# Kernel optimization log

Measured on AMD Instinct MI355X. Metric: run time of the kernel, lower is better.

The kernel has to match this reference:

```python
import jax, jax.numpy as jnp
import numpy as np

HEADS = 8
GROUPS = 32   # Group_cnt in the source
WIN = 16      # config.local_window_size


def _gn_nc(x, groups, eps):
    # group_norm on [N, C] (affine=False)
    N, C = x.shape
    xg = x.reshape(N, groups, C // groups)
    m = xg.mean(axis=2, keepdims=True)
    v = xg.var(axis=2, keepdims=True)
    return ((xg - m) / jnp.sqrt(v + eps)).reshape(N, C)


def _gn_nchw(x, groups, eps):
    # group_norm on [B, C, H, W] (affine=False)
    B, C, H, W = x.shape
    xg = x.reshape(B, groups, C // groups, H, W)
    m = xg.mean(axis=(2, 3, 4), keepdims=True)
    v = xg.var(axis=(2, 3, 4), keepdims=True)
    return ((xg - m) / jnp.sqrt(v + eps)).reshape(B, C, H, W)


def _conv3x3(x, w, b=None):
    y = jax.lax.conv_general_dilated(x, w, (1, 1), 'SAME',
                                     dimension_numbers=('NCHW', 'OIHW', 'NCHW'))
    return y if b is None else y + b[None, :, None, None]


def _forward(x, temb, conv1_w, conv1_b, conv2_w, g_diff, g_res, g2, g3,
             qkv2_w, qkv2_b, out2_w, qkv3_w, qkv3_b, out3_w,
             lsa_qkv_w, lsa_out_w):
    # ---- Residual_Block (layer1) ----
    h = _gn_nchw(x, GROUPS, 1e-6)
    h = _conv3x3(h, conv1_w, conv1_b)
    h = h + g_diff * temb[:, :, None, None]      # gate_diffusion (ReZero-style gate)
    h = jax.nn.silu(h)
    h = _gn_nchw(h, GROUPS, 1e-6)
    h = _conv3x3(h, conv2_w)
    h = _gn_nchw(h, GROUPS, 1e-6)
    x = x + g_res * h                            # gate_residual

    B, C, Fq, T = x.shape
    Dh = C // HEADS
    scale = 1.0 / jnp.sqrt(jnp.float32(Dh))      # (F/heads)**0.5 divisor

    # ---- SelfAttention over frequency axis (layer2): batch B*T, seq Fq ----
    xf = x.transpose(0, 3, 2, 1).reshape(B * T, Fq, C)
    qkv = xf @ qkv2_w + qkv2_b                   # [B*T, Fq, 3C]
    q, k, v = [t.reshape(B * T, Fq, HEADS, Dh) for t in jnp.split(qkv, 3, axis=-1)]
    p = jax.nn.softmax(jnp.einsum('bLhf,blhf->bLlh', q, k) * scale, axis=2)
    y = jnp.einsum('blhf,bLlh->bLhf', v, p).reshape(B * T, Fq, C) @ out2_w
    y = _gn_nc(y.reshape(-1, C), GROUPS, 1e-5).reshape(B * T, Fq, C)
    xf = xf + g2 * y                             # gate2

    # ---- GlobalAttention over time axis (layer3): batch B*Fq, seq T ----
    xt = xf.reshape(B, T, Fq, C).transpose(0, 2, 1, 3).reshape(B * Fq, T, C)
    qkv = xt @ qkv3_w + qkv3_b
    q, k, v = [t.reshape(B * Fq, T, HEADS, Dh) for t in jnp.split(qkv, 3, axis=-1)]
    p = jax.nn.softmax(jnp.einsum('bhf,blhf->blh', q.mean(axis=1), k) * scale, axis=1)
    y = jnp.einsum('blhf,blh->bhf', v, p).reshape(B * Fq, C) @ out3_w
    y = _gn_nc(y, GROUPS, 1e-5).reshape(B * Fq, 1, C)
    xt = xt + g3 * y                             # gate3, broadcast over T
    x = xt.reshape(B, Fq, T, C).transpose(0, 3, 1, 2)

    # ---- LSA_block (layer4): pre-norm local windowed attention along T, residual ----
    h = _gn_nchw(x, GROUPS, 1e-5)
    h = h.transpose(0, 2, 3, 1).reshape(B * Fq, T, C)
    nw = T // WIN
    qkv = (h @ lsa_qkv_w).reshape(B * Fq, nw, WIN, 3 * C)
    q, k, v = [t.reshape(B * Fq, nw, WIN, HEADS, Dh) for t in jnp.split(qkv, 3, axis=-1)]
    p = jax.nn.softmax(jnp.einsum('nwqhd,nwkhd->nwqkh', q, k) * scale, axis=3)
    o = jnp.einsum('nwqkh,nwkhd->nwqhd', p, v).reshape(B * Fq, T, C) @ lsa_out_w
    return x + o.reshape(B, Fq, T, C).transpose(0, 3, 1, 2)


def setup_inputs() -> dict:
    key = jax.random.key(0)
    ks = jax.random.split(key, 10)
    B, C, Fq, T = 4, 256, 64, 256
    w = lambda k, s: jax.random.normal(k, s, dtype=jnp.float32) * 0.02
    return {
        'x': jax.random.normal(ks[0], (B, C, Fq, T), dtype=jnp.float32),
        'temb': jax.random.normal(ks[1], (B, C), dtype=jnp.float32),
        'conv1_w': w(ks[2], (C, C, 3, 3)),
        'conv1_b': jnp.zeros((C,), jnp.float32),
        'conv2_w': w(ks[3], (C, C, 3, 3)),
        'g_diff': jnp.full((1,), 0.5, jnp.float32),
        'g_res': jnp.full((1,), 0.5, jnp.float32),
        'g2': jnp.full((1,), 0.5, jnp.float32),
        'g3': jnp.full((1,), 0.5, jnp.float32),
        'qkv2_w': w(ks[4], (C, 3 * C)),
        'qkv2_b': jnp.zeros((3 * C,), jnp.float32),
        'out2_w': w(ks[5], (C, C)),
        'qkv3_w': w(ks[6], (C, 3 * C)),
        'qkv3_b': jnp.zeros((3 * C,), jnp.float32),
        'out3_w': w(ks[7], (C, C)),
        'lsa_qkv_w': w(ks[8], (C, 3 * C)),
        'lsa_out_w': w(ks[9], (C, C)),
    }


def reference(x, temb, conv1_w, conv1_b, conv2_w, g_diff, g_res, g2, g3,
              qkv2_w, qkv2_b, out2_w, qkv3_w, qkv3_b, out3_w,
              lsa_qkv_w, lsa_out_w):
    return _forward(x, temb, conv1_w, conv1_b, conv2_w, g_diff, g_res, g2, g3,
                    qkv2_w, qkv2_b, out2_w, qkv3_w, qkv3_b, out3_w,
                    lsa_qkv_w, lsa_out_w)
```

## Files before the change

kernel.cpp:

```cpp
#include <hip/hip_runtime.h>

#define NN 16777216
#define CC 256
#define FF 64
#define TT 256

typedef short v8s __attribute__((ext_vector_type(8)));
typedef float v4f __attribute__((ext_vector_type(4)));

__device__ __forceinline__ unsigned short f2bf(float f) {
  unsigned u = __float_as_uint(f);
  u += 0x7fff + ((u >> 16) & 1);
  return (unsigned short)(u >> 16);
}
__device__ __forceinline__ float bf2f(unsigned short h) {
  return __uint_as_float(((unsigned)h) << 16);
}
__device__ __forceinline__ unsigned packbf2(float a, float b) {
  return (unsigned)f2bf(a) | ((unsigned)f2bf(b) << 16);
}
__device__ __forceinline__ void unpack8(uint4 u, float* d) {
  d[0] = __uint_as_float(u.x << 16); d[1] = __uint_as_float(u.x & 0xffff0000u);
  d[2] = __uint_as_float(u.y << 16); d[3] = __uint_as_float(u.y & 0xffff0000u);
  d[4] = __uint_as_float(u.z << 16); d[5] = __uint_as_float(u.z & 0xffff0000u);
  d[6] = __uint_as_float(u.w << 16); d[7] = __uint_as_float(u.w & 0xffff0000u);
}

__device__ __forceinline__ void blockReduce2(float& a, float& b, float* sbuf) {
  #pragma unroll
  for (int off = 32; off > 0; off >>= 1) {
    a += __shfl_down(a, off, 64);
    b += __shfl_down(b, off, 64);
  }
  int w = threadIdx.x >> 6;
  if ((threadIdx.x & 63) == 0) { sbuf[w] = a; sbuf[4 + w] = b; }
  __syncthreads();
  if (threadIdx.x == 0) {
    a = sbuf[0] + sbuf[1] + sbuf[2] + sbuf[3];
    b = sbuf[4] + sbuf[5] + sbuf[6] + sbuf[7];
  }
}

__global__ void prep_all_k(const float* __restrict__ c1w, const float* __restrict__ c2w,
    const float* __restrict__ q2w, const float* __restrict__ o2w, const float* __restrict__ q3w,
    const float* __restrict__ lqw, const float* __restrict__ low,
    unsigned short* __restrict__ WB1, unsigned short* __restrict__ WB2,
    unsigned short* __restrict__ Q2T, unsigned short* __restrict__ O2T,
    unsigned short* __restrict__ Q3T, unsigned short* __restrict__ LQT,
    unsigned short* __restrict__ LOT, float* __restrict__ stats) {
  long s = (long)blockIdx.x * 256 + threadIdx.x;
  if (s < 1024) { stats[s] = 0.f; return; }
  s -= 1024;
  if (s < 589824) {
    int co = (int)(s / 2304), r = (int)(s % 2304);
    int ci = r / 9, tap = r % 9;
    WB1[(tap * 256 + co) * 256 + ci] = f2bf(c1w[s]);
    return;
  }
  s -= 589824;
  if (s < 589824) {
    int co = (int)(s / 2304), r = (int)(s % 2304);
    int ci = r / 9, tap = r % 9;
    WB2[(tap * 256 + co) * 256 + ci] = f2bf(c2w[s]);
    return;
  }
  s -= 589824;
  if (s < 196608) { int k = (int)(s / 768), n = (int)(s % 768); Q2T[n * 256 + k] = f2bf(q2w[s]); return; }
  s -= 196608;
  if (s < 65536)  { int k = (int)(s / 256), n = (int)(s % 256); O2T[n * 256 + k] = f2bf(o2w[s]); return; }
  s -= 65536;
  if (s < 196608) { int k = (int)(s / 768), n = (int)(s % 768); Q3T[n * 256 + k] = f2bf(q3w[s]); return; }
  s -= 196608;
  if (s < 196608) { int k = (int)(s / 768), n = (int)(s % 768); LQT[n * 256 + k] = f2bf(lqw[s]); return; }
  s -= 196608;
  if (s < 65536)  { int k = (int)(s / 256), n = (int)(s % 256); LOT[n * 256 + k] = f2bf(low[s]); return; }
}

__global__ __launch_bounds__(256) void gn_stats_contig(const float* __restrict__ src, float* __restrict__ stats) {
  __shared__ float sbuf[8];
  int grp = blockIdx.x >> 3, chunk = blockIdx.x & 7;
  const float4* p = (const float4*)src + grp * 32768 + chunk * 4096;
  float s = 0.f, ss = 0.f;
  for (int i = threadIdx.x; i < 4096; i += 256) {
    float4 v = p[i];
    s += v.x + v.y + v.z + v.w;
    ss += v.x * v.x + v.y * v.y + v.z * v.z + v.w * v.w;
  }
  blockReduce2(s, ss, sbuf);
  if (threadIdx.x == 0) { atomicAdd(&stats[grp], s); atomicAdd(&stats[128 + grp], ss); }
}

__global__ __launch_bounds__(256) void gn_apply_tr_k(const float* __restrict__ src,
    const float* __restrict__ stats, unsigned short* __restrict__ XC, float eps) {
  __shared__ float sT[32][33];
  int bx = blockIdx.x;
  int r = bx >> 6;
  int c0 = ((bx >> 3) & 7) * 32;
  int t0 = (bx & 7) * 32;
  int b = r >> 6, f = r & 63;
  int tl = threadIdx.x & 31, tr = threadIdx.x >> 5;
  #pragma unroll
  for (int i = 0; i < 4; ++i) {
    int c = c0 + tr + i * 8;
    int grp = b * 32 + (c >> 3);
    float mean = stats[grp] * (1.f / 131072.f);
    float var = stats[128 + grp] * (1.f / 131072.f) - mean * mean;
    float rv = rsqrtf(var + eps);
    float v = src[((b * 256 + c) * 64 + f) * 256 + t0 + tl];
    sT[tr + i * 8][tl] = (v - mean) * rv;
  }
  __syncthreads();
  #pragma unroll
  for (int i = 0; i < 4; ++i) {
    int t = t0 + tr + i * 8;
    XC[(((size_t)(b * 64 + f)) * 256 + t) * 256 + c0 + tl] = f2bf(sT[tl][tr + i * 8]);
  }
}

__global__ __launch_bounds__(256) void gn_tr_resid_k(const float* __restrict__ h,
    const float* __restrict__ x, const float* __restrict__ stats,
    const float* __restrict__ gate, float* __restrict__ XF, float eps) {
  __shared__ float sT[32][33];
  int bx = blockIdx.x;
  int r = bx >> 6;
  int c0 = ((bx >> 3) & 7) * 32;
  int t0 = (bx & 7) * 32;
  int b = r >> 6, f = r & 63;
  int tl = threadIdx.x & 31, tr = threadIdx.x >> 5;
  float g = gate[0];
  #pragma unroll
  for (int i = 0; i < 4; ++i) {
    int c = c0 + tr + i * 8;
    int grp = b * 32 + (c >> 3);
    float mean = stats[grp] * (1.f / 131072.f);
    float var = stats[128 + grp] * (1.f / 131072.f) - mean * mean;
    float rv = rsqrtf(var + eps);
    int idx = ((b * 256 + c) * 64 + f) * 256 + t0 + tl;
    sT[tr + i * 8][tl] = x[idx] + g * (h[idx] - mean) * rv;
  }
  __syncthreads();
  #pragma unroll
  for (int i = 0; i < 4; ++i) {
    int t = t0 + tr + i * 8;
    XF[(((size_t)(b * 256 + t)) * 64 + f) * 256 + c0 + tl] = sT[tl][tr + i * 8];
  }
}

__global__ __launch_bounds__(256, 4) void conv3x3_mfma_k(const unsigned short* __restrict__ XC,
    const unsigned short* __restrict__ wb, const float* __restrict__ bias,
    const float* __restrict__ temb, const float* __restrict__ gd,
    float* __restrict__ out, float* __restrict__ ostats, int mode) {
  __shared__ __align__(16) unsigned short sIn[258][40];
  __shared__ __align__(16) unsigned short sW[3][64][40];
  int f  = blockIdx.x;
  int b  = blockIdx.y >> 2;
  int co0 = (blockIdx.y & 3) * 64;
  int tid = threadIdx.x;
  int wave = tid >> 6, lane = tid & 63;
  int lm = lane & 15, quad = lane >> 4;
  int w64 = wave * 64;
  v4f acc[4][4];
  #pragma unroll
  for (int i = 0; i < 4; ++i)
    #pragma unroll
    for (int j = 0; j < 4; ++j) acc[i][j] = (v4f)(0.f);

  for (int ci0 = 0; ci0 < 256; ci0 += 32) {
    for (int df = 0; df < 3; ++df) {
      __syncthreads();
      for (int s = tid; s < 1032; s += 256) {
        int tl = s >> 2, part = s & 3;
        int fi = f + df - 1, tg = tl - 1;
        uint4 val = make_uint4(0, 0, 0, 0);
        if (fi >= 0 && fi < 64 && tg >= 0 && tg < 256)
          val = *(const uint4*)&XC[(((size_t)(b * 64 + fi)) * 256 + tg) * 256 + ci0 + part * 8];
        *(uint4*)&sIn[tl][part * 8] = val;
      }
      for (int s = tid; s < 768; s += 256) {
        int tap3 = s >> 8, r = s & 255;
        int co = r >> 2, part = r & 3;
        *(uint4*)&sW[tap3][co][part * 8] =
            *(const uint4*)&wb[((size_t)((df * 3 + tap3) * 256) + co0 + co) * 256 + ci0 + part * 8];
      }
      __syncthreads();
      #pragma unroll
      for (int dt = 0; dt < 3; ++dt) {
        v8s A[4];
        #pragma unroll
        for (int mt = 0; mt < 4; ++mt)
          A[mt] = *(const v8s*)&sIn[w64 + mt * 16 + lm + dt][quad * 8];
        #pragma unroll
        for (int nt = 0; nt < 4; ++nt) {
          v8s B = *(const v8s*)&sW[dt][nt * 16 + lm][quad * 8];
          #pragma unroll
          for (int mt = 0; mt < 4; ++mt)
            acc[mt][nt] = __builtin_amdgcn_mfma_f32_16x16x32_bf16(A[mt], B, acc[mt][nt], 0, 0, 0);
        }
      }
    }
  }
  __syncthreads();
  float* sStat = (float*)sIn;
  float gdv = mode ? gd[0] : 0.f;
  float sch, qch;
  #pragma unroll
  for (int nt = 0; nt < 4; ++nt) {
    int co = co0 + nt * 16 + lm;
    float bb = 0.f;
    if (mode) bb = bias[co] + gdv * temb[b * 256 + co];
    sch = 0.f; qch = 0.f;
    #pragma unroll
    for (int mt = 0; mt < 4; ++mt) {
      int t = w64 + mt * 16 + quad * 4;
      float v0 = acc[mt][nt][0] + bb, v1 = acc[mt][nt][1] + bb;
      float v2 = acc[mt][nt][2] + bb, v3 = acc[mt][nt][3] + bb;
      if (mode) {
        v0 = v0 / (1.f + expf(-v0)); v1 = v1 / (1.f + expf(-v1));
        v2 = v2 / (1.f + expf(-v2)); v3 = v3 / (1.f + expf(-v3));
      }
      float4 o; o.x = v0; o.y = v1; o.z = v2; o.w = v3;
      *(float4*)&out[(((size_t)b * 256 + co) * 64 + f) * 256 + t] = o;
      sch += v0 + v1 + v2 + v3;
      qch += v0 * v0 + v1 * v1 + v2 * v2 + v3 * v3;
    }
    sch += __shfl_xor(sch, 16); qch += __shfl_xor(qch, 16);
    sch += __shfl_xor(sch, 32); qch += __shfl_xor(qch, 32);
    if (quad == 0) {
      sStat[((wave * 4 + nt) * 16 + lm) * 2]     = sch;
      sStat[((wave * 4 + nt) * 16 + lm) * 2 + 1] = qch;
    }
  }
  __syncthreads();
  if (tid < 64) {
    int c = tid;
    int nt = c >> 4, lmm = c & 15;
    float s = 0.f, q = 0.f;
    #pragma unroll
    for (int w = 0; w < 4; ++w) {
      s += sStat[((w * 4 + nt) * 16 + lmm) * 2];
      q += sStat[((w * 4 + nt) * 16 + lmm) * 2 + 1];
    }
    s += __shfl_xor(s, 1); q += __shfl_xor(q, 1);
    s += __shfl_xor(s, 2); q += __shfl_xor(q, 2);
    s += __shfl_xor(s, 4); q += __shfl_xor(q, 4);
    if ((c & 7) == 0) {
      int g = (co0 + c) >> 3;
      atomicAdd(&ostats[b * 32 + g], s);
      atomicAdd(&ostats[128 + b * 32 + g], q);
    }
  }
}

__global__ __launch_bounds__(256) void gemm_af32_k(const float* __restrict__ A, int lda,
    const unsigned short* __restrict__ BT, const float* __restrict__ bias,
    unsigned short* __restrict__ Cb, int ldc,
    const float* __restrict__ gstats, int growbase, float eps) {
  __shared__ __align__(16) unsigned short sA[128][40];
  __shared__ __align__(16) unsigned short sB[128][40];
  int n0 = blockIdx.x * 128, m0 = blockIdx.y * 128;
  int tid = threadIdx.x;
  int wave = tid >> 6, lane = tid & 63;
  int wm = wave >> 1, wn = wave & 1;
  int lm = lane & 15, quad = lane >> 4;
  v4f acc[4][4];
  #pragma unroll
  for (int i = 0; i < 4; ++i)
    #pragma unroll
    for (int j = 0; j < 4; ++j) acc[i][j] = (v4f)(0.f);

  for (int k0 = 0; k0 < 256; k0 += 32) {
    __syncthreads();
    #pragma unroll
    for (int i = 0; i < 4; ++i) {
      int s = tid + i * 256;
      int row = s >> 3, k4 = s & 7;
      float4 av = *(const float4*)&A[(size_t)(m0 + row) * lda + k0 + k4 * 4];
      if (gstats) {
        int grp = ((growbase + m0 + row) >> 14) * 32 + ((k0 + k4 * 4) >> 3);
        float mean = gstats[grp] * (1.f / 131072.f);
        float var = gstats[128 + grp] * (1.f / 131072.f) - mean * mean;
        float rr = rsqrtf(var + eps);
        av.x = (av.x - mean) * rr; av.y = (av.y - mean) * rr;
        av.z = (av.z - mean) * rr; av.w = (av.w - mean) * rr;
      }
      *(uint2*)&sA[row][k4 * 4] = make_uint2(packbf2(av.x, av.y), packbf2(av.z, av.w));
    }
    #pragma unroll
    for (int i = 0; i < 2; ++i) {
      int s = tid + i * 256;
      int n = s >> 2, part = s & 3;
      *(uint4*)&sB[n][part * 8] = *(const uint4*)&BT[(size_t)(n0 + n) * 256 + k0 + part * 8];
    }
    __syncthreads();
    v8s Af[4];
    #pragma unroll
    for (int mt = 0; mt < 4; ++mt)
      Af[mt] = *(const v8s*)&sA[wm * 64 + mt * 16 + lm][quad * 8];
    #pragma unroll
    for (int nt = 0; nt < 4; ++nt) {
      v8s Bf = *(const v8s*)&sB[wn * 64 + nt * 16 + lm][quad * 8];
      #pragma unroll
      for (int mt = 0; mt < 4; ++mt)
        acc[mt][nt] = __builtin_amdgcn_mfma_f32_16x16x32_bf16(Af[mt], Bf, acc[mt][nt], 0, 0, 0);
    }
  }
  #pragma unroll
  for (int nt = 0; nt < 4; ++nt) {
    int col = n0 + wn * 64 + nt * 16 + lm;
    float bb = bias ? bias[col] : 0.f;
    #pragma unroll
    for (int mt = 0; mt < 4; ++mt) {
      int row = m0 + wm * 64 + mt * 16 + quad * 4;
      #pragma unroll
      for (int r = 0; r < 4; ++r)
        Cb[(size_t)(row + r) * ldc + col] = f2bf(acc[mt][nt][r] + bb);
    }
  }
}

__global__ __launch_bounds__(256) void gemm_abf16_k(const unsigned short* __restrict__ A, int lda,
    const unsigned short* __restrict__ BT,
    const float* __restrict__ xfin, float* __restrict__ xtout, int rowbase,
    unsigned short* __restrict__ Cb, int ldc, const float* __restrict__ gate) {
  __shared__ __align__(16) unsigned short sA[128][40];
  __shared__ __align__(16) unsigned short sB[128][40];
  int n0 = blockIdx.x * 128, m0 = blockIdx.y * 128;
  int tid = threadIdx.x;
  int wave = tid >> 6, lane = tid & 63;
  int wm = wave >> 1, wn = wave & 1;
  int lm = lane & 15, quad = lane >> 4;
  v4f acc[4][4];
  #pragma unroll
  for (int i = 0; i < 4; ++i)
    #pragma unroll
    for (int j = 0; j < 4; ++j) acc[i][j] = (v4f)(0.f);

  for (int k0 = 0; k0 < 256; k0 += 32) {
    __syncthreads();
    #pragma unroll
    for (int i = 0; i < 2; ++i) {
      int s = tid + i * 256;
      int row = s >> 2, part = s & 3;
      *(uint4*)&sA[row][part * 8] = *(const uint4*)&A[(size_t)(m0 + row) * lda + k0 + part * 8];
      *(uint4*)&sB[row][part * 8] = *(const uint4*)&BT[(size_t)(n0 + row) * 256 + k0 + part * 8];
    }
    __syncthreads();
    v8s Af[4];
    #pragma unroll
    for (int mt = 0; mt < 4; ++mt)
      Af[mt] = *(const v8s*)&sA[wm * 64 + mt * 16 + lm][quad * 8];
    #pragma unroll
    for (int nt = 0; nt < 4; ++nt) {
      v8s Bf = *(const v8s*)&sB[wn * 64 + nt * 16 + lm][quad * 8];
      #pragma unroll
      for (int mt = 0; mt < 4; ++mt)
        acc[mt][nt] = __builtin_amdgcn_mfma_f32_16x16x32_bf16(Af[mt], Bf, acc[mt][nt], 0, 0, 0);
    }
  }
  if (xtout) {
    float g = gate[0];
    #pragma unroll
    for (int mt = 0; mt < 4; ++mt) {
      int rowb = m0 + wm * 64 + mt * 16 + quad * 4;
      #pragma unroll
      for (int r = 0; r < 4; ++r) {
        int rowl = rowb + r;
        int rowg = rowbase + rowl;
        int b = rowg >> 14, t = (rowg >> 6) & 255, fq = rowg & 63;
        size_t xtrow = (size_t)((b * 64 + fq) * 256 + t) * 256;
        #pragma unroll
        for (int nt = 0; nt < 4; ++nt) {
          float v = acc[mt][nt][r];
          float s = v, q = v * v;
          s += __shfl_xor(s, 1); q += __shfl_xor(q, 1);
          s += __shfl_xor(s, 2); q += __shfl_xor(q, 2);
          s += __shfl_xor(s, 4); q += __shfl_xor(q, 4);
          float m = s * 0.125f;
          float var = q * 0.125f - m * m;
          float norm = (v - m) * rsqrtf(var + 1e-5f);
          int col = n0 + wn * 64 + nt * 16 + lm;
          xtout[xtrow + col] = xfin[(size_t)rowl * 256 + col] + g * norm;
        }
      }
    }
  } else {
    #pragma unroll
    for (int nt = 0; nt < 4; ++nt) {
      int col = n0 + wn * 64 + nt * 16 + lm;
      #pragma unroll
      for (int mt = 0; mt < 4; ++mt) {
        int row = m0 + wm * 64 + mt * 16 + quad * 4;
        #pragma unroll
        for (int r = 0; r < 4; ++r)
          Cb[(size_t)(row + r) * ldc + col] = f2bf(acc[mt][nt][r]);
      }
    }
  }
}

__global__ __launch_bounds__(256) void gemm_k(const float* __restrict__ A, int lda,
    const float* __restrict__ Bm, int N, const float* __restrict__ bias,
    float* __restrict__ Cm, int ldc, int gn) {
  __shared__ __align__(16) float sA[16][64];
  __shared__ __align__(16) float sB[16][64];
  int n0 = blockIdx.x * 64, m0 = blockIdx.y * 64;
  int tid = threadIdx.x;
  int tx = tid & 15, ty = tid >> 4;
  int arow = m0 + (tid >> 2), acol = (tid & 3) * 4;
  int brow = tid >> 4, bcol = (tid & 15) * 4;
  float acc[4][4] = {};
  for (int k0 = 0; k0 < 256; k0 += 16) {
    __syncthreads();
    float4 av = *(const float4*)&A[(size_t)arow * lda + k0 + acol];
    sA[acol + 0][tid >> 2] = av.x;
    sA[acol + 1][tid >> 2] = av.y;
    sA[acol + 2][tid >> 2] = av.z;
    sA[acol + 3][tid >> 2] = av.w;
    *(float4*)&sB[brow][bcol] = *(const float4*)&Bm[(k0 + brow) * N + n0 + bcol];
    __syncthreads();
    #pragma unroll
    for (int kk = 0; kk < 16; ++kk) {
      float4 a = *(const float4*)&sA[kk][ty * 4];
      float4 b = *(const float4*)&sB[kk][tx * 4];
      float aa[4] = {a.x, a.y, a.z, a.w};
      float bb[4] = {b.x, b.y, b.z, b.w};
      #pragma unroll
      for (int i = 0; i < 4; ++i)
        #pragma unroll
        for (int j = 0; j < 4; ++j)
          acc[i][j] += aa[i] * bb[j];
    }
  }
  #pragma unroll
  for (int i = 0; i < 4; ++i) {
    float m = 0.f, rv = 1.f;
    if (gn) {
      float s = acc[i][0] + acc[i][1] + acc[i][2] + acc[i][3];
      float q = acc[i][0] * acc[i][0] + acc[i][1] * acc[i][1]
              + acc[i][2] * acc[i][2] + acc[i][3] * acc[i][3];
      s += __shfl_xor(s, 1); q += __shfl_xor(q, 1);
      m = s * 0.125f;
      float var = q * 0.125f - m * m;
      rv = rsqrtf(var + 1e-5f);
    }
    #pragma unroll
    for (int j = 0; j < 4; ++j) {
      int n = n0 + tx * 4 + j;
      float v = acc[i][j];
      if (gn) v = (v - m) * rv;
      else if (bias) v += bias[n];
      Cm[(size_t)(m0 + ty * 4 + i) * ldc + n] = v;
    }
  }
}

__global__ __launch_bounds__(256) void final_out_k(const float* __restrict__ XT,
    const unsigned short* __restrict__ O2b, float* __restrict__ out, int rbase) {
  __shared__ float sT[32][33];
  int bx = blockIdx.x;
  int rl = bx >> 6;
  int t0 = ((bx >> 3) & 7) * 32;
  int c0 = (bx & 7) * 32;
  int rg = rbase + rl;
  int b = rg >> 6, f = rg & 63;
  int tc = threadIdx.x & 31, tr = threadIdx.x >> 5;
  #pragma unroll
  for (int i = 0; i < 4; ++i) {
    int t = t0 + tr + i * 8;
    sT[tr + i * 8][tc] = XT[(size_t)rg * 65536 + t * 256 + c0 + tc]
                       + bf2f(O2b[(size_t)rl * 65536 + t * 256 + c0 + tc]);
  }
  __syncthreads();
  #pragma unroll
  for (int i = 0; i < 4; ++i) {
    int c = c0 + tr + i * 8;
    out[((b * CC + c) * FF + f) * TT + t0 + tc] = sT[tc][tr + i * 8];
  }
}

__global__ __launch_bounds__(256) void attn2_mfma_k(unsigned short* __restrict__ Q) {
  __shared__ __align__(16) unsigned short sP[4][64][72];
  __shared__ __align__(16) unsigned short sVt[4][32][72];
  int bt = blockIdx.x;
  int tid = threadIdx.x;
  int wave = tid >> 6, lane = tid & 63;
  int lm = lane & 15, quad = lane >> 4;
  const float scale = 0.17677669529663687f;
  size_t rowbase = (size_t)bt * 64;
  unsigned short (*P)[72] = sP[wave];
  unsigned short (*Vt)[72] = sVt[wave];
  #pragma unroll
  for (int hh = 0; hh < 2; ++hh) {
    int h = wave * 2 + hh;
    int hoff = h * 32;
    v8s Af[4], Bf[4];
    #pragma unroll
    for (int mt = 0; mt < 4; ++mt)
      Af[mt] = *(const v8s*)&Q[(rowbase + mt * 16 + lm) * 768 + hoff + quad * 8];
    #pragma unroll
    for (int nt = 0; nt < 4; ++nt)
      Bf[nt] = *(const v8s*)&Q[(rowbase + nt * 16 + lm) * 768 + 256 + hoff + quad * 8];
    v4f S[4][4];
    #pragma unroll
    for (int mt = 0; mt < 4; ++mt)
      #pragma unroll
      for (int nt = 0; nt < 4; ++nt)
        S[mt][nt] = __builtin_amdgcn_mfma_f32_16x16x32_bf16(Af[mt], Bf[nt], (v4f)(0.f), 0, 0, 0);
    #pragma unroll
    for (int part = 0; part < 4; ++part) {
      uint4 u = *(const uint4*)&Q[(rowbase + lane) * 768 + 512 + hoff + part * 8];
      unsigned short* up = (unsigned short*)&u;
      #pragma unroll
      for (int j = 0; j < 8; ++j) Vt[part * 8 + j][lane] = up[j];
    }
    float inv[4][4];
    #pragma unroll
    for (int mt = 0; mt < 4; ++mt) {
      #pragma unroll
      for (int r = 0; r < 4; ++r) {
        float v0 = S[mt][0][r] * scale, v1 = S[mt][1][r] * scale;
        float v2 = S[mt][2][r] * scale, v3 = S[mt][3][r] * scale;
        float mx = fmaxf(fmaxf(v0, v1), fmaxf(v2, v3));
        mx = fmaxf(mx, __shfl_xor(mx, 1));
        mx = fmaxf(mx, __shfl_xor(mx, 2));
        mx = fmaxf(mx, __shfl_xor(mx, 4));
        mx = fmaxf(mx, __shfl_xor(mx, 8));
        float e0 = __expf(v0 - mx), e1 = __expf(v1 - mx);
        float e2 = __expf(v2 - mx), e3 = __expf(v3 - mx);
        float sm = e0 + e1 + e2 + e3;
        sm += __shfl_xor(sm, 1);
        sm += __shfl_xor(sm, 2);
        sm += __shfl_xor(sm, 4);
        sm += __shfl_xor(sm, 8);
        inv[mt][r] = 1.f / sm;
        int row = mt * 16 + quad * 4 + r;
        P[row][lm]      = f2bf(e0);
        P[row][16 + lm] = f2bf(e1);
        P[row][32 + lm] = f2bf(e2);
        P[row][48 + lm] = f2bf(e3);
      }
    }
    v8s Ap[4][2], Bv[2][2];
    #pragma unroll
    for (int mt = 0; mt < 4; ++mt)
      #pragma unroll
      for (int kc = 0; kc < 2; ++kc)
        Ap[mt][kc] = *(const v8s*)&P[mt * 16 + lm][kc * 32 + quad * 8];
    #pragma unroll
    for (int nd = 0; nd < 2; ++nd)
      #pragma unroll
      for (int kc = 0; kc < 2; ++kc)
        Bv[nd][kc] = *(const v8s*)&Vt[nd * 16 + lm][kc * 32 + quad * 8];
    #pragma unroll
    for (int mt = 0; mt < 4; ++mt) {
      #pragma unroll
      for (int nd = 0; nd < 2; ++nd) {
        v4f O = (v4f)(0.f);
        O = __builtin_amdgcn_mfma_f32_16x16x32_bf16(Ap[mt][0], Bv[nd][0], O, 0, 0, 0);
        O = __builtin_amdgcn_mfma_f32_16x16x32_bf16(Ap[mt][1], Bv[nd][1], O, 0, 0, 0);
        #pragma unroll
        for (int r = 0; r < 4; ++r)
          P[mt * 16 + quad * 4 + r][nd * 16 + lm] = f2bf(O[r] * inv[mt][r]);
      }
    }
    #pragma unroll
    for (int part = 0; part < 4; ++part) {
      uint4 u = *(const uint4*)&P[lane][part * 8];
      *(uint4*)&Q[(rowbase + lane) * 768 + hoff + part * 8] = u;
    }
  }
}

__global__ __launch_bounds__(256) void attn3_k(const unsigned short* __restrict__ Q3,
                                               float* __restrict__ y3, int bf_base) {
  __shared__ float sQp[64][33];
  __shared__ float sqm[32];
  __shared__ float sp[256];
  __shared__ float sred[256];
  int bfl = blockIdx.x >> 3, h = blockIdx.x & 7;
  int tid = threadIdx.x;
  int tq = tid >> 2, c4 = tid & 3;
  int d8 = c4 * 8;
  const float scale = 0.17677669529663687f;
  size_t rowbase = (size_t)bfl * 256;
  {
    float a[8] = {};
    #pragma unroll
    for (int i = 0; i < 4; ++i) {
      int t = i * 64 + tq;
      float v[8];
      unpack8(*(const uint4*)&Q3[(rowbase + t) * 768 + h * 32 + d8], v);
      #pragma unroll
      for (int j = 0; j < 8; ++j) a[j] += v[j];
    }
    #pragma unroll
    for (int j = 0; j < 8; ++j) sQp[tq][d8 + j] = a[j];
  }
  __syncthreads();
  if (tid < 32) {
    float m = 0.f;
    for (int g = 0; g < 64; ++g) m += sQp[g][tid];
    sqm[tid] = m * (1.f / 256.f);
  }
  __syncthreads();
  {
    float dot = 0.f;
    #pragma unroll
    for (int p = 0; p < 4; ++p) {
      float v[8];
      unpack8(*(const uint4*)&Q3[(rowbase + tid) * 768 + 256 + h * 32 + p * 8], v);
      #pragma unroll
      for (int j = 0; j < 8; ++j) dot += sqm[p * 8 + j] * v[j];
    }
    sp[tid] = dot * scale;
    sred[tid] = sp[tid];
  }
  __syncthreads();
  for (int st = 128; st > 0; st >>= 1) { if (tid < st) sred[tid] = fmaxf(sred[tid], sred[tid + st]); __syncthreads(); }
  float mx = sred[0];
  __syncthreads();
  float e = expf(sp[tid] - mx);
  sred[tid] = e;
  __syncthreads();
  for (int st = 128; st > 0; st >>= 1) { if (tid < st) sred[tid] += sred[tid + st]; __syncthreads(); }
  float rinv = 1.f / sred[0];
  sp[tid] = e * rinv;
  __syncthreads();
  {
    float a[8] = {};
    #pragma unroll
    for (int i = 0; i < 4; ++i) {
      int t = i * 64 + tq;
      float w = sp[t];
      float v[8];
      unpack8(*(const uint4*)&Q3[(rowbase + t) * 768 + 512 + h * 32 + d8], v);
      #pragma unroll
      for (int j = 0; j < 8; ++j) a[j] += w * v[j];
    }
    #pragma unroll
    for (int j = 0; j < 8; ++j) sQp[tq][d8 + j] = a[j];
  }
  __syncthreads();
  if (tid < 32) {
    float o = 0.f;
    for (int g = 0; g < 64; ++g) o += sQp[g][tid];
    y3[(size_t)(bf_base + bfl) * 256 + h * 32 + tid] = o;
  }
}

__global__ __launch_bounds__(256) void lsa_attn_k(unsigned short* __restrict__ Q4) {
  __shared__ __align__(16) float sX[16][772];
  __shared__ float sS[8][16][17];
  __shared__ float sInv[8][16];
  int bfl = blockIdx.x >> 4, w = blockIdx.x & 15;
  int tid = threadIdx.x;
  size_t rb = ((size_t)(bfl * 256 + w * 16)) * 768;
  for (int s = tid; s < 1536; s += 256) {
    int t = s / 96, c8 = (s - t * 96) * 8;
    unpack8(*(const uint4*)&Q4[rb + t * 768 + c8], &sX[t][c8]);
  }
  __syncthreads();
  const float scale = 0.17677669529663687f;
  #pragma unroll
  for (int rep = 0; rep < 8; ++rep) {
    int idx = tid + rep * 256;
    int h = idx >> 8, q = (idx >> 4) & 15, k = idx & 15;
    float dot = 0.f;
    const float* qp = &sX[q][h * 32];
    const float* kp = &sX[k][256 + h * 32];
    for (int d = 0; d < 32; ++d) dot += qp[d] * kp[d];
    sS[h][q][k] = dot * scale;
  }
  __syncthreads();
  if (tid < 128) {
    int h = tid >> 4, q = tid & 15;
    float mx = -1e30f;
    for (int k = 0; k < 16; ++k) mx = fmaxf(mx, sS[h][q][k]);
    float sum = 0.f;
    for (int k = 0; k < 16; ++k) { float e = expf(sS[h][q][k] - mx); sS[h][q][k] = e; sum += e; }
    sInv[h][q] = 1.f / sum;
  }
  __syncthreads();
  #pragma unroll
  for (int rep = 0; rep < 8; ++rep) {
    int idx = tid + rep * 256;
    int t = idx >> 7, c2 = (idx & 127) * 2;
    int h = c2 >> 5;
    float a0 = 0.f, a1 = 0.f;
    for (int k = 0; k < 16; ++k) {
      float p = sS[h][t][k];
      a0 += p * sX[k][512 + c2];
      a1 += p * sX[k][512 + c2 + 1];
    }
    float riv = sInv[h][t];
    *(unsigned*)&Q4[rb + t * 768 + c2] = packbf2(a0 * riv, a1 * riv);
  }
}

__global__ __launch_bounds__(256) void bcast_add_k(float* __restrict__ XT, const float* __restrict__ y3n,
                                                   const float* __restrict__ gate) {
  int i4 = blockIdx.x * 256 + threadIdx.x;
  int flat = i4 * 4;
  int r = flat >> 16, c = flat & 255;
  float g = gate[0];
  float4 v = ((float4*)XT)[i4];
  float4 a = *(const float4*)&y3n[r * 256 + c];
  v.x += g * a.x; v.y += g * a.y; v.z += g * a.z; v.w += g * a.w;
  ((float4*)XT)[i4] = v;
}

__global__ __launch_bounds__(256) void gn_stats_xt_k(const float* __restrict__ X, float* __restrict__ stats) {
  __shared__ float sbuf[8];
  int bx = blockIdx.x;
  int b = bx >> 11, g = (bx >> 6) & 31, f = bx & 63;
  size_t base = (size_t)(b * 64 + f) * 65536 + g * 8;
  float s = 0.f, ss = 0.f;
  for (int i = threadIdx.x; i < 2048; i += 256) {
    int t = i >> 3, c = i & 7;
    float v = X[base + t * 256 + c];
    s += v; ss += v * v;
  }
  blockReduce2(s, ss, sbuf);
  if (threadIdx.x == 0) { atomicAdd(&stats[b * 32 + g], s); atomicAdd(&stats[128 + b * 32 + g], ss); }
}

extern "C" void kernel_launch(void* const* d_in, const int* in_sizes, int n_in,
                              void* d_out, int out_size, void* d_ws, size_t ws_size,
                              hipStream_t stream) {
  (void)in_sizes; (void)n_in; (void)out_size;
  const float* x        = (const float*)d_in[0];
  const float* temb     = (const float*)d_in[1];
  const float* conv1_w  = (const float*)d_in[2];
  const float* conv1_b  = (const float*)d_in[3];
  const float* conv2_w  = (const float*)d_in[4];
  const float* g_diff   = (const float*)d_in[5];
  const float* g_res    = (const float*)d_in[6];
  const float* g2       = (const float*)d_in[7];
  const float* g3       = (const float*)d_in[8];
  const float* qkv2_w   = (const float*)d_in[9];
  const float* qkv2_b   = (const float*)d_in[10];
  const float* out2_w   = (const float*)d_in[11];
  const float* qkv3_w   = (const float*)d_in[12];
  const float* qkv3_b   = (const float*)d_in[13];
  const float* out3_w   = (const float*)d_in[14];
  const float* lsa_qkv_w = (const float*)d_in[15];
  const float* lsa_out_w = (const float*)d_in[16];
  float* out = (float*)d_out;
  float* ws = (float*)d_ws;

  int NCHv = 4;
  {
    auto need = [](int nch) -> size_t {
      size_t rows = 65536 / nch;
      size_t uslots = rows * 512;
      if (uslots < 8388608) uslots = 8388608;
      return 4ull * ((size_t)NN + uslots + 950272 + 198000);
    };
    if (ws_size >= need(1)) NCHv = 1;
    else if (ws_size >= need(2)) NCHv = 2;
  }
  const size_t rows = 65536 / NCHv;

  float* W = ws;
  float* U = ws + (size_t)NN;
  unsigned short* XC  = (unsigned short*)U;
  unsigned short* QB  = (unsigned short*)U;
  unsigned short* O2B = (unsigned short*)(U + rows * 384);
  size_t uslots = rows * 512; if (uslots < 8388608) uslots = 8388608;
  float* WREG = U + uslots;
  unsigned short* WB1   = (unsigned short*)WREG;
  unsigned short* WB2   = WB1 + 589824;
  unsigned short* QKV2T = WB2 + 589824;
  unsigned short* OUT2T = QKV2T + 196608;
  unsigned short* QKV3T = OUT2T + 65536;
  unsigned short* LSAQT = QKV3T + 196608;
  unsigned short* LSAOT = LSAQT + 196608;
  float* Y3    = WREG + 950272;
  float* Y3O   = Y3 + 65536;
  float* Y3N   = Y3O + 65536;
  float* STATS = Y3N + 65536;
  float* ST0 = STATS, *ST1 = STATS + 256, *ST2 = STATS + 512, *ST3 = STATS + 768;
  float* D = out;

  dim3 b256(256);
  prep_all_k<<<7428, b256, 0, stream>>>(conv1_w, conv2_w, qkv2_w, out2_w, qkv3_w,
                                        lsa_qkv_w, lsa_out_w,
                                        WB1, WB2, QKV2T, OUT2T, QKV3T, LSAQT, LSAOT, STATS);

  gn_stats_contig<<<1024, b256, 0, stream>>>(x, ST0);
  gn_apply_tr_k<<<16384, b256, 0, stream>>>(x, ST0, XC, 1e-6f);
  conv3x3_mfma_k<<<dim3(64, 16), b256, 0, stream>>>(XC, WB1, conv1_b, temb, g_diff, W, ST1, 1);
  gn_apply_tr_k<<<16384, b256, 0, stream>>>(W, ST1, XC, 1e-6f);
  conv3x3_mfma_k<<<dim3(64, 16), b256, 0, stream>>>(XC, WB2, nullptr, nullptr, nullptr, W, ST2, 0);
  gn_tr_resid_k<<<16384, b256, 0, stream>>>(W, x, ST2, g_res, D, 1e-6f);

  for (int c = 0; c < NCHv; ++c) {
    float* XFr = D + (size_t)c * rows * 256;
    gemm_af32_k<<<dim3(6, rows / 128), b256, 0, stream>>>(XFr, 256, QKV2T, qkv2_b, QB, 768, nullptr, 0, 0.f);
    attn2_mfma_k<<<rows / 64, b256, 0, stream>>>(QB);
    gemm_abf16_k<<<dim3(2, rows / 128), b256, 0, stream>>>(QB, 768, OUT2T,
                                                           XFr, W, (int)(c * rows),
                                                           nullptr, 256, g2);
  }

  for (int c = 0; c < NCHv; ++c) {
    const float* XTr = W + (size_t)c * rows * 256;
    gemm_af32_k<<<dim3(6, rows / 128), b256, 0, stream>>>(XTr, 256, QKV3T, qkv3_b, QB, 768, nullptr, 0, 0.f);
    attn3_k<<<(rows / 256) * 8, b256, 0, stream>>>(QB, Y3, c * (int)(rows / 256));
  }
  gemm_k<<<dim3(4, 4), b256, 0, stream>>>(Y3, 256, out3_w, 256, nullptr, Y3N, 256, 1);
  bcast_add_k<<<16384, b256, 0, stream>>>(W, Y3N, g3);

  gn_stats_xt_k<<<8192, b256, 0, stream>>>(W, ST3);
  for (int c = 0; c < NCHv; ++c) {
    const float* XTr = W + (size_t)c * rows * 256;
    gemm_af32_k<<<dim3(6, rows / 128), b256, 0, stream>>>(XTr, 256, LSAQT, nullptr, QB, 768,
                                                          ST3, (int)(c * rows), 1e-5f);
    lsa_attn_k<<<(rows / 256) * 16, b256, 0, stream>>>(QB);
    gemm_abf16_k<<<dim3(2, rows / 128), b256, 0, stream>>>(QB, 768, LSAOT,
                                                           nullptr, nullptr, 0,
                                                           O2B, 256, nullptr);
    final_out_k<<<(rows / 256) * 64, b256, 0, stream>>>(W, O2B, out, c * (int)(rows / 256));
  }
}
```

Before: 1.060 ms.

## Fuse final residual add and transpose into LSA output GEMM; rewrite GN stats

The LSA output projection GEMM now adds the XT residual and writes straight to the NCHW output in its epilogue. This removes the bf16 intermediate buffer and the separate final_out_k transpose kernel. The group-norm statistics kernel over XT is rewritten to stream contiguous float4 rows with far fewer blocks, replacing strided 8-wide reads. The fused epilogue's scattered stores to the transposed output (stride of T across columns) may coalesce poorly. Output is also no longer rounded to bf16 before the add.

After: 1.005 ms. 5.2% less time.

```diff
diff --git a/kernel.cpp b/kernel.cpp
--- a/kernel.cpp
+++ b/kernel.cpp
@@ -321,7 +321,7 @@
 __global__ __launch_bounds__(256) void gemm_abf16_k(const unsigned short* __restrict__ A, int lda,
     const unsigned short* __restrict__ BT,
     const float* __restrict__ xfin, float* __restrict__ xtout, int rowbase,
-    unsigned short* __restrict__ Cb, int ldc, const float* __restrict__ gate) {
+    unsigned short* __restrict__ Cb, int ldc, const float* __restrict__ gate, int mode) {
   __shared__ __align__(16) unsigned short sA[128][40];
   __shared__ __align__(16) unsigned short sB[128][40];
   int n0 = blockIdx.x * 128, m0 = blockIdx.y * 128;
@@ -357,7 +357,7 @@
         acc[mt][nt] = __builtin_amdgcn_mfma_f32_16x16x32_bf16(Af[mt], Bf, acc[mt][nt], 0, 0, 0);
     }
   }
-  if (xtout) {
+  if (mode == 1) {
     float g = gate[0];
     #pragma unroll
     for (int mt = 0; mt < 4; ++mt) {
@@ -380,6 +380,23 @@
           float norm = (v - m) * rsqrtf(var + 1e-5f);
           int col = n0 + wn * 64 + nt * 16 + lm;
           xtout[xtrow + col] = xfin[(size_t)rowl * 256 + col] + g * norm;
+        }
+      }
+    }
+  } else if (mode == 2) {
+    #pragma unroll
+    for (int mt = 0; mt < 4; ++mt) {
+      int rowb = m0 + wm * 64 + mt * 16 + quad * 4;
+      #pragma unroll
+      for (int r = 0; r < 4; ++r) {
+        int rowl = rowb + r;
+        int rowg = rowbase + rowl;
+        int b = rowg >> 14, fq = (rowg >> 8) & 63, t = rowg & 255;
+        #pragma unroll
+        for (int nt = 0; nt < 4; ++nt) {
+          int col = n0 + wn * 64 + nt * 16 + lm;
+          float v = acc[mt][nt][r] + xfin[(size_t)rowl * 256 + col];
+          xtout[(((size_t)b * 256 + col) * 64 + fq) * 256 + t] = v;
         }
       }
     }
@@ -451,30 +468,6 @@
       else if (bias) v += bias[n];
       Cm[(size_t)(m0 + ty * 4 + i) * ldc + n] = v;
     }
-  }
-}
-
-__global__ __launch_bounds__(256) void final_out_k(const float* __restrict__ XT,
-    const unsigned short* __restrict__ O2b, float* __restrict__ out, int rbase) {
-  __shared__ float sT[32][33];
-  int bx = blockIdx.x;
-  int rl = bx >> 6;
-  int t0 = ((bx >> 3) & 7) * 32;
-  int c0 = (bx & 7) * 32;
-  int rg = rbase + rl;
-  int b = rg >> 6, f = rg & 63;
-  int tc = threadIdx.x & 31, tr = threadIdx.x >> 5;
-  #pragma unroll
-  for (int i = 0; i < 4; ++i) {
-    int t = t0 + tr + i * 8;
-    sT[tr + i * 8][tc] = XT[(size_t)rg * 65536 + t * 256 + c0 + tc]
-                       + bf2f(O2b[(size_t)rl * 65536 + t * 256 + c0 + tc]);
-  }
-  __syncthreads();
-  #pragma unroll
-  for (int i = 0; i < 4; ++i) {
-    int c = c0 + tr + i * 8;
-    out[((b * CC + c) * FF + f) * TT + t0 + tc] = sT[tc][tr + i * 8];
   }
 }
 
@@ -709,19 +702,33 @@
   ((float4*)XT)[i4] = v;
 }
 
-__global__ __launch_bounds__(256) void gn_stats_xt_k(const float* __restrict__ X, float* __restrict__ stats) {
-  __shared__ float sbuf[8];
-  int bx = blockIdx.x;
-  int b = bx >> 11, g = (bx >> 6) & 31, f = bx & 63;
-  size_t base = (size_t)(b * 64 + f) * 65536 + g * 8;
-  float s = 0.f, ss = 0.f;
-  for (int i = threadIdx.x; i < 2048; i += 256) {
-    int t = i >> 3, c = i & 7;
-    float v = X[base + t * 256 + c];
-    s += v; ss += v * v;
-  }
-  blockReduce2(s, ss, sbuf);
-  if (threadIdx.x == 0) { atomicAdd(&stats[b * 32 + g], s); atomicAdd(&stats[128 + b * 32 + g], ss); }
+__global__ __launch_bounds__(256) void gn_stats_xt2_k(const float* __restrict__ X, float* __restrict__ stats) {
+  __shared__ float sacc[4][64];
+  int bf = blockIdx.x >> 1, half = blockIdx.x & 1;
+  int b = bf >> 6;
+  int tid = threadIdx.x;
+  const float4* p = (const float4*)X + (size_t)bf * 16384 + half * 8192;
+  float s = 0.f, q = 0.f;
+  #pragma unroll 4
+  for (int k = 0; k < 32; ++k) {
+    float4 v = p[tid + k * 256];
+    s += v.x + v.y + v.z + v.w;
+    q += v.x * v.x + v.y * v.y + v.z * v.z + v.w * v.w;
+  }
+  s += __shfl_xor(s, 1); q += __shfl_xor(q, 1);
+  int lane = tid & 63, wave = tid >> 6;
+  if ((lane & 1) == 0) {
+    int g = (lane >> 1) & 31;
+    sacc[wave][g * 2] = s;
+    sacc[wave][g * 2 + 1] = q;
+  }
+  __syncthreads();
+  if (tid < 64) {
+    int g = tid >> 1, isq = tid & 1;
+    float acc = sacc[0][g * 2 + isq] + sacc[1][g * 2 + isq]
+              + sacc[2][g * 2 + isq] + sacc[3][g * 2 + isq];
+    atomicAdd(&stats[isq * 128 + b * 32 + g], acc);
+  }
 }
 
 extern "C" void kernel_launch(void* const* d_in, const int* in_sizes, int n_in,
@@ -766,6 +773,7 @@
   unsigned short* XC  = (unsigned short*)U;
   unsigned short* QB  = (unsigned short*)U;
   unsigned short* O2B = (unsigned short*)(U + rows * 384);
+  (void)O2B;
   size_t uslots = rows * 512; if (uslots < 8388608) uslots = 8388608;
   float* WREG = U + uslots;
   unsigned short* WB1   = (unsigned short*)WREG;
@@ -800,7 +808,7 @@
     attn2_mfma_k<<<rows / 64, b256, 0, stream>>>(QB);
     gemm_abf16_k<<<dim3(2, rows / 128), b256, 0, stream>>>(QB, 768, OUT2T,
                                                            XFr, W, (int)(c * rows),
-                                                           nullptr, 256, g2);
+                                                           nullptr, 256, g2, 1);
   }
 
   for (int c = 0; c < NCHv; ++c) {
@@ -811,15 +819,14 @@
   gemm_k<<<dim3(4, 4), b256, 0, stream>>>(Y3, 256, out3_w, 256, nullptr, Y3N, 256, 1);
   bcast_add_k<<<16384, b256, 0, stream>>>(W, Y3N, g3);
 
-  gn_stats_xt_k<<<8192, b256, 0, stream>>>(W, ST3);
+  gn_stats_xt2_k<<<512, b256, 0, stream>>>(W, ST3);
   for (int c = 0; c < NCHv; ++c) {
     const float* XTr = W + (size_t)c * rows * 256;
     gemm_af32_k<<<dim3(6, rows / 128), b256, 0, stream>>>(XTr, 256, LSAQT, nullptr, QB, 768,
                                                           ST3, (int)(c * rows), 1e-5f);
     lsa_attn_k<<<(rows / 256) * 16, b256, 0, stream>>>(QB);
     gemm_abf16_k<<<dim3(2, rows / 128), b256, 0, stream>>>(QB, 768, LSAOT,
-                                                           nullptr, nullptr, 0,
-                                                           O2B, 256, nullptr);
-    final_out_k<<<(rows / 256) * 64, b256, 0, stream>>>(W, O2B, out, c * (int)(rows / 256));
-  }
-}
+                                                           XTr, out, (int)(c * rows),
+                                                           nullptr, 256, nullptr, 2);
+  }
+}
```
